# Kernel tuning notes

Hardware: AMD Instinct MI355X
Metric: run time of the kernel (lower is better)

The kernel has to match this reference:

```python
import jax, jax.numpy as jnp
import numpy as np

C = 256
G = 32  # groups
EPS = 1e-5

def _xavier(key, shape, gain=1.0):
    fan_in, fan_out = shape[1], shape[0]
    a = gain * np.sqrt(6.0 / (fan_in + fan_out))
    return jax.random.uniform(key, shape, jnp.float32, -a, a)

def setup_inputs() -> dict:
    key = jax.random.key(0)
    ks = jax.random.split(key, 5)
    x = jax.random.normal(ks[0], (2, C, 16, 16, 16), jnp.float32)
    return {
        "x": x,
        "gn_gamma": jnp.ones((C,), jnp.float32),
        "gn_beta": jnp.zeros((C,), jnp.float32),
        "Wq": _xavier(ks[1], (C, C)), "bq": jnp.zeros((C,), jnp.float32),
        "Wk": _xavier(ks[2], (C, C)), "bk": jnp.zeros((C,), jnp.float32),
        "Wv": _xavier(ks[3], (C, C)), "bv": jnp.zeros((C,), jnp.float32),
        "Wp": _xavier(ks[4], (C, C), gain=1e-05), "bp": jnp.zeros((C,), jnp.float32),
    }

def reference(x, gn_gamma, gn_beta, Wq, bq, Wk, bk, Wv, bv, Wp, bp):
    B, Cc, D, H, W = x.shape
    N = D * H * W
    xf = x.reshape(B, Cc, N)  # [B, C, N]
    # GroupNorm over (C//G, N) per group
    xg = xf.reshape(B, G, Cc // G, N)
    mu = jnp.mean(xg, axis=(2, 3), keepdims=True)
    var = jnp.var(xg, axis=(2, 3), keepdims=True)
    h = ((xg - mu) * jax.lax.rsqrt(var + EPS)).reshape(B, Cc, N)
    h = h * gn_gamma[None, :, None] + gn_beta[None, :, None]
    # 1x1x1 convs == channel matmuls
    q = jnp.einsum('oc,bcn->bno', Wq, h) + bq  # [B, N, C]
    k = jnp.einsum('oc,bcn->bon', Wk, h) + bk[None, :, None]  # [B, C, N]
    v = jnp.einsum('oc,bcn->bno', Wv, h) + bv  # [B, N, C]
    scale = float(Cc) ** (-0.5)
    w = jnp.einsum('bnc,bcm->bnm', q, k) * scale  # [B, N, N]
    w = jax.nn.softmax(w, axis=-1)
    a = jnp.einsum('bnm,bmc->bnc', w, v)  # [B, N, C]
    out = jnp.einsum('oc,bnc->bon', Wp, a) + bp[None, :, None]  # [B, C, N]
    return x + out.reshape(B, Cc, D, H, W)
```

## Files before the change

kernel.cpp:

```cpp
#include <hip/hip_runtime.h>
#include <stdint.h>

#define B_ 2
#define C_ 256
#define N_ 4096
#define EPS_ 1e-5f

typedef short short8 __attribute__((ext_vector_type(8)));
typedef float f32x4 __attribute__((ext_vector_type(4)));
typedef float f32x16 __attribute__((ext_vector_type(16)));
typedef long long i64;

static __device__ __forceinline__ unsigned short f2bf(float f) {
    union { float f; unsigned int u; } v; v.f = f;
    unsigned int r = v.u + 0x7FFF + ((v.u >> 16) & 1);
    return (unsigned short)(r >> 16);
}
static __device__ __forceinline__ float bf2f(unsigned short u) {
    union { unsigned int u; float f; } v; v.u = ((unsigned int)u) << 16;
    return v.f;
}
static __device__ __forceinline__ unsigned char f2fp8(float f) {
    return (unsigned char)(__builtin_amdgcn_cvt_pk_fp8_f32(f, f, 0, false) & 0xff);
}
static __device__ __forceinline__ unsigned short pk_bf8(float a, float b) {
    return (unsigned short)(__builtin_amdgcn_cvt_pk_bf8_f32(a, b, 0, false) & 0xffff);
}

__global__ __launch_bounds__(256) void prep(
    const float* __restrict__ x, float2* __restrict__ stats,
    const float* __restrict__ Wq, const float* __restrict__ Wk,
    const float* __restrict__ Wv, const float* __restrict__ Wp,
    ushort* __restrict__ o)
{
    __shared__ float as_[4], as2_[4];
    if (blockIdx.x < 64) {
        const float4* p = reinterpret_cast<const float4*>(x + (size_t)blockIdx.x * 32768);
        float s = 0.f, ss = 0.f;
        for (int i = threadIdx.x; i < 8192; i += 256) {
            float4 v = p[i];
            s  += v.x + v.y + v.z + v.w;
            ss += v.x*v.x + v.y*v.y + v.z*v.z + v.w*v.w;
        }
        for (int m = 32; m; m >>= 1) { s += __shfl_down(s, m, 64); ss += __shfl_down(ss, m, 64); }
        int w = threadIdx.x >> 6;
        if ((threadIdx.x & 63) == 0) { as_[w] = s; as2_[w] = ss; }
        __syncthreads();
        if (threadIdx.x == 0) {
            float S = as_[0]+as_[1]+as_[2]+as_[3], SS = as2_[0]+as2_[1]+as2_[2]+as2_[3];
            float mu = S / 32768.f;
            float var = SS / 32768.f - mu*mu;
            stats[blockIdx.x] = make_float2(mu, rsqrtf(var + EPS_));
        }
    } else {
        int t = (blockIdx.x - 64) * 256 + threadIdx.x;
        int idx = t * 4;
        int sel = idx >> 16;
        const float* src = sel == 0 ? Wq : sel == 1 ? Wk : sel == 2 ? Wv : Wp;
        float4 v = *reinterpret_cast<const float4*>(src + (idx & 65535));
        ushort4 r; r.x = f2bf(v.x); r.y = f2bf(v.y); r.z = f2bf(v.z); r.w = f2bf(v.w);
        *reinterpret_cast<ushort4*>(o + idx) = r;
    }
}

__global__ void gnorm_t(const float* __restrict__ x, const float2* __restrict__ stats,
                        const float* __restrict__ gamma, const float* __restrict__ beta,
                        ushort* __restrict__ ht) {
    __shared__ float tile[32][33];
    int b = blockIdx.z, n0 = blockIdx.x * 32, c0 = blockIdx.y * 32;
    int tx = threadIdx.x, ty = threadIdx.y;
    #pragma unroll
    for (int i = 0; i < 4; i++) {
        int c = c0 + ty + i*8;
        float2 st = stats[b*32 + (c >> 3)];
        float v = x[((size_t)(b*C_ + c))*N_ + n0 + tx];
        tile[ty + i*8][tx] = (v - st.x) * st.y * gamma[c] + beta[c];
    }
    __syncthreads();
    #pragma unroll
    for (int i = 0; i < 4; i++) {
        int n = n0 + ty + i*8;
        ht[((size_t)(b*N_ + n))*C_ + c0 + tx] = f2bf(tile[tx][ty + i*8]);
    }
}

__global__ __launch_bounds__(256) void qkvproj(
    const ushort* __restrict__ ht, const ushort* __restrict__ wq,
    const ushort* __restrict__ wk, const ushort* __restrict__ wv,
    const float* __restrict__ bq, const float* __restrict__ bk, const float* __restrict__ bv,
    unsigned char* __restrict__ qo, unsigned char* __restrict__ ko, unsigned char* __restrict__ vo)
{
    __shared__ ushort sA[64][72], sBq[64][72], sBk[64][72], sBv[64][72];
    int bz = blockIdx.z;
    const ushort* Ab = ht + (size_t)bz * N_ * C_;
    int i0 = blockIdx.x * 64, j0 = blockIdx.y * 64;
    int tid = threadIdx.x, w = tid >> 6, lane = tid & 63, lr = lane & 15, lg = lane >> 4;
    f32x4 aq[4] = {}, ak[4] = {}, av[4] = {};
    for (int ks = 0; ks < 256; ks += 64) {
        #pragma unroll
        for (int it = 0; it < 2; it++) {
            int ch = tid + it*256;
            int row = ch >> 3, cc = ch & 7;
            *reinterpret_cast<uint4*>(&sA[row][cc*8]) =
                *reinterpret_cast<const uint4*>(Ab + ((size_t)(i0 + row))*256 + ks + cc*8);
            *reinterpret_cast<uint4*>(&sBq[row][cc*8]) =
                *reinterpret_cast<const uint4*>(wq + ((size_t)(j0 + row))*256 + ks + cc*8);
            *reinterpret_cast<uint4*>(&sBk[row][cc*8]) =
                *reinterpret_cast<const uint4*>(wk + ((size_t)(j0 + row))*256 + ks + cc*8);
            *reinterpret_cast<uint4*>(&sBv[row][cc*8]) =
                *reinterpret_cast<const uint4*>(wv + ((size_t)(j0 + row))*256 + ks + cc*8);
        }
        __syncthreads();
        #pragma unroll
        for (int kc = 0; kc < 2; kc++) {
            short8 af = *reinterpret_cast<const short8*>(&sA[w*16 + lr][kc*32 + lg*8]);
            #pragma unroll
            for (int cb = 0; cb < 4; cb++) {
                short8 b1 = *reinterpret_cast<const short8*>(&sBq[cb*16 + lr][kc*32 + lg*8]);
                short8 b2 = *reinterpret_cast<const short8*>(&sBk[cb*16 + lr][kc*32 + lg*8]);
                short8 b3 = *reinterpret_cast<const short8*>(&sBv[cb*16 + lr][kc*32 + lg*8]);
                aq[cb] = __builtin_amdgcn_mfma_f32_16x16x32_bf16(af, b1, aq[cb], 0, 0, 0);
                ak[cb] = __builtin_amdgcn_mfma_f32_16x16x32_bf16(af, b2, ak[cb], 0, 0, 0);
                av[cb] = __builtin_amdgcn_mfma_f32_16x16x32_bf16(af, b3, av[cb], 0, 0, 0);
            }
        }
        __syncthreads();
    }
    #pragma unroll
    for (int cb = 0; cb < 4; cb++) {
        #pragma unroll
        for (int r = 0; r < 4; r++) {
            int i = i0 + w*16 + lg*4 + r;
            int j = j0 + cb*16 + lr;
            size_t oidx = ((size_t)(bz*N_ + i))*256 + j;
            qo[oidx] = f2fp8(aq[cb][r] + bq[j]);
            ko[oidx] = f2fp8(ak[cb][r] + bk[j]);
            int m = i & 63;
            int col = (i & ~63) + ((m & 31)*2 + (m >> 5));
            vo[((size_t)bz*C_ + j)*N_ + col] = f2fp8(av[cb][r] + bv[j]);
        }
    }
}

#define FLASH_LDS 79872
__global__ __launch_bounds__(256, 2) void flash5(
    const unsigned char* __restrict__ q, const unsigned char* __restrict__ k,
    const unsigned char* __restrict__ vT,
    ushort* __restrict__ Opart, float* __restrict__ lsum, ushort* __restrict__ aout, int nsplit)
{
    extern __shared__ char smem[];
    int b = blockIdx.z, s = blockIdx.y, qt = blockIdx.x;
    int tid = threadIdx.x, w = tid >> 6, lane = tid & 63;
    int l31 = lane & 31, hi = lane >> 5;
    int nrow0 = qt*128 + w*32;
    const unsigned char* kB = k  + (size_t)b * N_ * 256;
    const unsigned char* vB = vT + (size_t)b * 256 * N_;

    i64 qf[16];
    #pragma unroll
    for (int kc = 0; kc < 16; kc++)
        qf[kc] = *reinterpret_cast<const i64*>(
            q + ((size_t)(b*N_) + nrow0 + l31)*256 + kc*16 + hi*8);

    f32x16 oacc[8] = {};
    float lpart[16] = {};

    int tiles = 64 / nsplit;
    int t0 = s * tiles;

    char* kbuf0 = smem;
    char* vbuf0 = smem + 33792;
    char* pw    = smem + 70656 + w*2304;

    uint4 kreg[4], vreg[4];
    auto loadKV = [&](int t) {
        #pragma unroll
        for (int i = 0; i < 4; i++) {
            int row = w*16 + i*4 + (lane >> 4);
            kreg[i] = *reinterpret_cast<const uint4*>(
                kB + (size_t)(t*64 + row)*256 + (lane & 15)*16);
        }
        #pragma unroll
        for (int i = 0; i < 4; i++) {
            int c = w*64 + i*16 + (lane >> 2);
            vreg[i] = *reinterpret_cast<const uint4*>(
                vB + (size_t)c*4096 + t*64 + (lane & 3)*16);
        }
    };
    auto writeKV = [&](int sel) {
        #pragma unroll
        for (int i = 0; i < 4; i++) {
            int row = w*16 + i*4 + (lane >> 4);
            char* p = kbuf0 + sel*16896 + row*264 + (lane & 15)*16;
            *reinterpret_cast<uint2*>(p)     = make_uint2(kreg[i].x, kreg[i].y);
            *reinterpret_cast<uint2*>(p + 8) = make_uint2(kreg[i].z, kreg[i].w);
        }
        #pragma unroll
        for (int i = 0; i < 4; i++) {
            int c = w*64 + i*16 + (lane >> 2);
            char* p = vbuf0 + sel*18432 + c*72 + (lane & 3)*16;
            *reinterpret_cast<uint2*>(p)     = make_uint2(vreg[i].x, vreg[i].y);
            *reinterpret_cast<uint2*>(p + 8) = make_uint2(vreg[i].z, vreg[i].w);
        }
    };

    loadKV(t0);
    writeKV(0);
    __syncthreads();
    int sel = 0;

    for (int ti = 0; ti < tiles; ti++) {
        int t = t0 + ti;
        int tn = (ti + 1 < tiles) ? t + 1 : t0;
        loadKV(tn);

        const char* kb_ = kbuf0 + sel*16896;
        f32x16 s0 = {}, s1 = {};
        __builtin_amdgcn_s_setprio(1);
        #pragma unroll
        for (int kc = 0; kc < 16; kc++) {
            i64 b0 = *reinterpret_cast<const i64*>(kb_ + l31*264        + kc*16 + hi*8);
            i64 b1 = *reinterpret_cast<const i64*>(kb_ + (l31+32)*264   + kc*16 + hi*8);
            s0 = __builtin_amdgcn_mfma_f32_32x32x16_fp8_fp8(qf[kc], b0, s0, 0, 0, 0);
            s1 = __builtin_amdgcn_mfma_f32_32x32x16_fp8_fp8(qf[kc], b1, s1, 0, 0, 0);
        }
        __builtin_amdgcn_s_setprio(0);

        #pragma unroll
        for (int r = 0; r < 16; r++) {
            int R = (r & 3) + 8*(r >> 2) + 4*hi;
            float p0 = __expf(fminf(s0[r]*0.0625f, 10.5f));
            float p1 = __expf(fminf(s1[r]*0.0625f, 10.5f));
            lpart[r] += p0 + p1;
            *(ushort*)(pw + R*72 + l31*2) = pk_bf8(p0, p1);
        }

        const char* vb_ = vbuf0 + sel*18432;
        i64 pa[4];
        #pragma unroll
        for (int ks = 0; ks < 4; ks++)
            pa[ks] = *reinterpret_cast<const i64*>(pw + l31*72 + ks*16 + hi*8);
        __builtin_amdgcn_s_setprio(1);
        #pragma unroll
        for (int cb = 0; cb < 8; cb++) {
            #pragma unroll
            for (int ks = 0; ks < 4; ks++) {
                i64 bv = *reinterpret_cast<const i64*>(vb_ + (cb*32 + l31)*72 + ks*16 + hi*8);
                oacc[cb] = __builtin_amdgcn_mfma_f32_32x32x16_bf8_fp8(pa[ks], bv, oacc[cb], 0, 0, 0);
            }
        }
        __builtin_amdgcn_s_setprio(0);

        writeKV(sel ^ 1);
        __syncthreads();
        sel ^= 1;
    }

    #pragma unroll
    for (int r = 0; r < 16; r++) {
        float v = lpart[r];
        v += __shfl_xor(v, 1, 64);
        v += __shfl_xor(v, 2, 64);
        v += __shfl_xor(v, 4, 64);
        v += __shfl_xor(v, 8, 64);
        v += __shfl_xor(v, 16, 64);
        lpart[r] = v;
    }

    if (nsplit == 1) {
        #pragma unroll
        for (int r = 0; r < 16; r++) {
            int R = (r & 3) + 8*(r >> 2) + 4*hi;
            float inv = 1.f / lpart[r];
            #pragma unroll
            for (int cb = 0; cb < 8; cb++)
                aout[((size_t)(b*N_) + nrow0 + R)*256 + cb*32 + l31] = f2bf(oacc[cb][r] * inv);
        }
    } else {
        size_t obase = ((size_t)(b*nsplit + s)*N_ + nrow0) * 256;
        #pragma unroll
        for (int r = 0; r < 16; r++) {
            int R = (r & 3) + 8*(r >> 2) + 4*hi;
            #pragma unroll
            for (int cb = 0; cb < 8; cb++)
                Opart[obase + (size_t)R*256 + cb*32 + l31] = f2bf(oacc[cb][r]);
        }
        if (l31 == 0) {
            #pragma unroll
            for (int r = 0; r < 16; r++)
                lsum[(size_t)(b*nsplit + s)*N_ + nrow0 + (r & 3) + 8*(r >> 2) + 4*hi] = lpart[r];
        }
    }
}

__global__ void combine2(const ushort* __restrict__ Opart, const float* __restrict__ lsum,
                         ushort* __restrict__ aout, int nsplit) {
    int g = threadIdx.x >> 6, lane = threadIdx.x & 63;
    int idx = blockIdx.x*4 + g;
    int b = idx >> 12, n = idx & 4095;
    float L = 0.f;
    for (int s2 = 0; s2 < nsplit; s2++) L += lsum[(size_t)(b*nsplit + s2)*N_ + n];
    float inv = 1.f / L;
    float a0 = 0.f, a1 = 0.f, a2 = 0.f, a3 = 0.f;
    for (int s2 = 0; s2 < nsplit; s2++) {
        ushort4 o = *reinterpret_cast<const ushort4*>(
            Opart + ((size_t)(b*nsplit + s2)*N_ + n)*256 + lane*4);
        a0 += bf2f(o.x); a1 += bf2f(o.y); a2 += bf2f(o.z); a3 += bf2f(o.w);
    }
    ushort4 r; r.x = f2bf(a0*inv); r.y = f2bf(a1*inv); r.z = f2bf(a2*inv); r.w = f2bf(a3*inv);
    *reinterpret_cast<ushort4*>(aout + (size_t)idx*256 + lane*4) = r;
}

__global__ __launch_bounds__(256) void pgemm(
    const ushort* __restrict__ A, const ushort* __restrict__ Bm,
    const float* __restrict__ bias, const float* __restrict__ resid,
    float* __restrict__ outp, long bBatch, long oBatch)
{
    __shared__ ushort sA[64][72];
    __shared__ ushort sB[64][72];
    int bz = blockIdx.z;
    const ushort* Bb = Bm + (size_t)bBatch * bz;
    int i0 = blockIdx.x * 64, j0 = blockIdx.y * 64;
    int tid = threadIdx.x, w = tid >> 6, lane = tid & 63, lr = lane & 15, lg = lane >> 4;
    f32x4 acc[4] = {};
    for (int ks = 0; ks < 256; ks += 64) {
        #pragma unroll
        for (int it = 0; it < 2; it++) {
            int ch = tid + it*256;
            int row = ch >> 3, cc = ch & 7;
            *reinterpret_cast<uint4*>(&sA[row][cc*8]) =
                *reinterpret_cast<const uint4*>(A + ((size_t)(i0 + row))*256 + ks + cc*8);
            *reinterpret_cast<uint4*>(&sB[row][cc*8]) =
                *reinterpret_cast<const uint4*>(Bb + ((size_t)(j0 + row))*256 + ks + cc*8);
        }
        __syncthreads();
        #pragma unroll
        for (int kc = 0; kc < 2; kc++) {
            short8 af = *reinterpret_cast<const short8*>(&sA[w*16 + lr][kc*32 + lg*8]);
            #pragma unroll
            for (int cb = 0; cb < 4; cb++) {
                short8 bf = *reinterpret_cast<const short8*>(&sB[cb*16 + lr][kc*32 + lg*8]);
                acc[cb] = __builtin_amdgcn_mfma_f32_16x16x32_bf16(af, bf, acc[cb], 0, 0, 0);
            }
        }
        __syncthreads();
    }
    #pragma unroll
    for (int cb = 0; cb < 4; cb++) {
        #pragma unroll
        for (int r = 0; r < 4; r++) {
            int i = i0 + w*16 + lg*4 + r;
            int j = j0 + cb*16 + lr;
            size_t oidx = (size_t)oBatch*bz + (size_t)i*N_ + j;
            outp[oidx] = acc[cb][r] + bias[i] + resid[oidx];
        }
    }
}

extern "C" void kernel_launch(void* const* d_in, const int* in_sizes, int n_in,
                              void* d_out, int out_size, void* d_ws, size_t ws_size,
                              hipStream_t stream) {
    const float* x     = (const float*)d_in[0];
    const float* gamma = (const float*)d_in[1];
    const float* beta  = (const float*)d_in[2];
    const float* Wq = (const float*)d_in[3]; const float* bq = (const float*)d_in[4];
    const float* Wk = (const float*)d_in[5]; const float* bk = (const float*)d_in[6];
    const float* Wv = (const float*)d_in[7]; const float* bv = (const float*)d_in[8];
    const float* Wp = (const float*)d_in[9]; const float* bp = (const float*)d_in[10];
    float* out = (float*)d_out;

    char* ws = (char*)d_ws;
    float2* stats = (float2*)ws;
    ushort* wqb = (ushort*)(ws + 1024);
    ushort* wkb = wqb + 65536;
    ushort* wvb = wkb + 65536;
    ushort* wpb = wvb + 65536;
    ushort* ht  = (ushort*)(ws + 1024 + 524288);
    const size_t NB = (size_t)B_ * N_ * C_;
    unsigned char* qb  = (unsigned char*)(ht + NB);
    unsigned char* kb8 = qb  + NB;
    unsigned char* vTb = kb8 + NB;
    ushort* ab = (ushort*)(vTb + NB);
    char* after = (char*)(ab + NB);
    float*  lsum  = (float*)after;
    ushort* Opart = (ushort*)(after + 262144);

    int nsplit = (ws_size >= (size_t)48*1024*1024) ? 8 : 4;

    hipFuncSetAttribute((const void*)flash5, hipFuncAttributeMaxDynamicSharedMemorySize,
                        FLASH_LDS);

    prep<<<320, 256, 0, stream>>>(x, stats, Wq, Wk, Wv, Wp, wqb);
    gnorm_t<<<dim3(128, 8, 2), dim3(32, 8), 0, stream>>>(x, stats, gamma, beta, ht);
    qkvproj<<<dim3(64, 4, 2), 256, 0, stream>>>(ht, wqb, wkb, wvb, bq, bk, bv, qb, kb8, vTb);
    flash5<<<dim3(32, nsplit, 2), 256, FLASH_LDS, stream>>>(qb, kb8, vTb, Opart, lsum, ab, nsplit);
    combine2<<<2048, 256, 0, stream>>>(Opart, lsum, ab, nsplit);
    pgemm<<<dim3(4, 64, 2), 256, 0, stream>>>(wpb, ab, bp, x, out, (long)N_*C_, (long)C_*N_);
}
```

Before: 84.47 us.

## Use 32x32x64 scaled f8f6f4 MFMA in flash attention with permuted K LDS layout

```diff
diff --git a/kernel.cpp b/kernel.cpp
--- a/kernel.cpp
+++ b/kernel.cpp
@@ -9,6 +9,7 @@
 typedef short short8 __attribute__((ext_vector_type(8)));
 typedef float f32x4 __attribute__((ext_vector_type(4)));
 typedef float f32x16 __attribute__((ext_vector_type(16)));
+typedef int i32x8 __attribute__((ext_vector_type(8)));
 typedef long long i64;
 
 static __device__ __forceinline__ unsigned short f2bf(float f) {
@@ -26,6 +27,9 @@
 static __device__ __forceinline__ unsigned short pk_bf8(float a, float b) {
     return (unsigned short)(__builtin_amdgcn_cvt_pk_bf8_f32(a, b, 0, false) & 0xffff);
 }
+
+union U32B { uint4 q[2]; i32x8 v; };
+union U32C { uint2 d[4]; i32x8 v; };
 
 __global__ __launch_bounds__(256) void prep(
     const float* __restrict__ x, float2* __restrict__ stats,
@@ -135,15 +139,13 @@
             size_t oidx = ((size_t)(bz*N_ + i))*256 + j;
             qo[oidx] = f2fp8(aq[cb][r] + bq[j]);
             ko[oidx] = f2fp8(ak[cb][r] + bk[j]);
-            int m = i & 63;
-            int col = (i & ~63) + ((m & 31)*2 + (m >> 5));
-            vo[((size_t)bz*C_ + j)*N_ + col] = f2fp8(av[cb][r] + bv[j]);
-        }
-    }
-}
-
-#define FLASH_LDS 79872
-__global__ __launch_bounds__(256, 2) void flash5(
+            vo[((size_t)bz*C_ + j)*N_ + i] = f2fp8(av[cb][r] + bv[j]);
+        }
+    }
+}
+
+#define FLASH_LDS 80896
+__global__ __launch_bounds__(256, 2) void flash6(
     const unsigned char* __restrict__ q, const unsigned char* __restrict__ k,
     const unsigned char* __restrict__ vT,
     ushort* __restrict__ Opart, float* __restrict__ lsum, ushort* __restrict__ aout, int nsplit)
@@ -156,11 +158,11 @@
     const unsigned char* kB = k  + (size_t)b * N_ * 256;
     const unsigned char* vB = vT + (size_t)b * 256 * N_;
 
-    i64 qf[16];
-    #pragma unroll
-    for (int kc = 0; kc < 16; kc++)
-        qf[kc] = *reinterpret_cast<const i64*>(
-            q + ((size_t)(b*N_) + nrow0 + l31)*256 + kc*16 + hi*8);
+    i32x8 qf[4];
+    #pragma unroll
+    for (int ks = 0; ks < 4; ks++)
+        qf[ks] = *reinterpret_cast<const i32x8*>(
+            q + ((size_t)(b*N_) + nrow0 + l31)*256 + ks*64 + hi*32);
 
     f32x16 oacc[8] = {};
     float lpart[16] = {};
@@ -168,61 +170,60 @@
     int tiles = 64 / nsplit;
     int t0 = s * tiles;
 
-    char* kbuf0 = smem;
-    char* vbuf0 = smem + 33792;
-    char* pw    = smem + 70656 + w*2304;
+    char* kls = smem;
+    char* vls = smem + 34816;
+    char* pw  = smem + 71680 + w*2304;
+
+    int koff[4], kd[4], voff[4], vd[4];
+    #pragma unroll
+    for (int i = 0; i < 4; i++) {
+        int row = w*16 + i*4 + (lane >> 4);
+        koff[i] = (t0*64 + row)*256 + (lane & 15)*16;
+        int pr = (row & 1)*32 + (row >> 1);
+        kd[i]  = pr*272 + (lane & 15)*16;
+        int c = w*64 + i*16 + (lane >> 2);
+        voff[i] = c*4096 + t0*64 + (lane & 3)*16;
+        vd[i]   = c*72 + (lane & 3)*16;
+    }
 
     uint4 kreg[4], vreg[4];
-    auto loadKV = [&](int t) {
-        #pragma unroll
-        for (int i = 0; i < 4; i++) {
-            int row = w*16 + i*4 + (lane >> 4);
-            kreg[i] = *reinterpret_cast<const uint4*>(
-                kB + (size_t)(t*64 + row)*256 + (lane & 15)*16);
-        }
-        #pragma unroll
-        for (int i = 0; i < 4; i++) {
-            int c = w*64 + i*16 + (lane >> 2);
-            vreg[i] = *reinterpret_cast<const uint4*>(
-                vB + (size_t)c*4096 + t*64 + (lane & 3)*16);
-        }
+    auto loadKV = [&]() {
+        #pragma unroll
+        for (int i = 0; i < 4; i++) { kreg[i] = *reinterpret_cast<const uint4*>(kB + koff[i]); koff[i] += 16384; }
+        #pragma unroll
+        for (int i = 0; i < 4; i++) { vreg[i] = *reinterpret_cast<const uint4*>(vB + voff[i]); voff[i] += 64; }
     };
     auto writeKV = [&](int sel) {
         #pragma unroll
-        for (int i = 0; i < 4; i++) {
-            int row = w*16 + i*4 + (lane >> 4);
-            char* p = kbuf0 + sel*16896 + row*264 + (lane & 15)*16;
-            *reinterpret_cast<uint2*>(p)     = make_uint2(kreg[i].x, kreg[i].y);
-            *reinterpret_cast<uint2*>(p + 8) = make_uint2(kreg[i].z, kreg[i].w);
-        }
-        #pragma unroll
-        for (int i = 0; i < 4; i++) {
-            int c = w*64 + i*16 + (lane >> 2);
-            char* p = vbuf0 + sel*18432 + c*72 + (lane & 3)*16;
-            *reinterpret_cast<uint2*>(p)     = make_uint2(vreg[i].x, vreg[i].y);
-            *reinterpret_cast<uint2*>(p + 8) = make_uint2(vreg[i].z, vreg[i].w);
-        }
+        for (int i = 0; i < 4; i++) *reinterpret_cast<uint4*>(kls + sel*17408 + kd[i]) = kreg[i];
+        #pragma unroll
+        for (int i = 0; i < 4; i++) *reinterpret_cast<uint4*>(vls + sel*18432 + vd[i]) = vreg[i];
     };
 
-    loadKV(t0);
+    loadKV();
     writeKV(0);
     __syncthreads();
     int sel = 0;
 
     for (int ti = 0; ti < tiles; ti++) {
-        int t = t0 + ti;
-        int tn = (ti + 1 < tiles) ? t + 1 : t0;
-        loadKV(tn);
-
-        const char* kb_ = kbuf0 + sel*16896;
+        bool more = (ti + 1 < tiles);
+        if (more) loadKV();
+
+        const char* kb_ = kls + sel*17408;
         f32x16 s0 = {}, s1 = {};
         __builtin_amdgcn_s_setprio(1);
         #pragma unroll
-        for (int kc = 0; kc < 16; kc++) {
-            i64 b0 = *reinterpret_cast<const i64*>(kb_ + l31*264        + kc*16 + hi*8);
-            i64 b1 = *reinterpret_cast<const i64*>(kb_ + (l31+32)*264   + kc*16 + hi*8);
-            s0 = __builtin_amdgcn_mfma_f32_32x32x16_fp8_fp8(qf[kc], b0, s0, 0, 0, 0);
-            s1 = __builtin_amdgcn_mfma_f32_32x32x16_fp8_fp8(qf[kc], b1, s1, 0, 0, 0);
+        for (int ks = 0; ks < 4; ks++) {
+            int off = ks*64 + hi*32;
+            U32B b0, b1;
+            b0.q[0] = *reinterpret_cast<const uint4*>(kb_ + l31*272 + off);
+            b0.q[1] = *reinterpret_cast<const uint4*>(kb_ + l31*272 + off + 16);
+            b1.q[0] = *reinterpret_cast<const uint4*>(kb_ + (l31+32)*272 + off);
+            b1.q[1] = *reinterpret_cast<const uint4*>(kb_ + (l31+32)*272 + off + 16);
+            s0 = __builtin_amdgcn_mfma_scale_f32_32x32x64_f8f6f4(
+                     qf[ks], b0.v, s0, 0, 0, 0, 127, 0, 127);
+            s1 = __builtin_amdgcn_mfma_scale_f32_32x32x64_f8f6f4(
+                     qf[ks], b1.v, s1, 0, 0, 0, 127, 0, 127);
         }
         __builtin_amdgcn_s_setprio(0);
 
@@ -235,23 +236,27 @@
             *(ushort*)(pw + R*72 + l31*2) = pk_bf8(p0, p1);
         }
 
-        const char* vb_ = vbuf0 + sel*18432;
-        i64 pa[4];
-        #pragma unroll
-        for (int ks = 0; ks < 4; ks++)
-            pa[ks] = *reinterpret_cast<const i64*>(pw + l31*72 + ks*16 + hi*8);
+        U32C pa;
+        pa.d[0] = *reinterpret_cast<const uint2*>(pw + l31*72 + hi*32);
+        pa.d[1] = *reinterpret_cast<const uint2*>(pw + l31*72 + hi*32 + 8);
+        pa.d[2] = *reinterpret_cast<const uint2*>(pw + l31*72 + hi*32 + 16);
+        pa.d[3] = *reinterpret_cast<const uint2*>(pw + l31*72 + hi*32 + 24);
+        const char* vb_ = vls + sel*18432;
         __builtin_amdgcn_s_setprio(1);
         #pragma unroll
         for (int cb = 0; cb < 8; cb++) {
-            #pragma unroll
-            for (int ks = 0; ks < 4; ks++) {
-                i64 bv = *reinterpret_cast<const i64*>(vb_ + (cb*32 + l31)*72 + ks*16 + hi*8);
-                oacc[cb] = __builtin_amdgcn_mfma_f32_32x32x16_bf8_fp8(pa[ks], bv, oacc[cb], 0, 0, 0);
-            }
+            const char* pv = vb_ + (cb*32 + l31)*72 + hi*32;
+            U32C bv;
+            bv.d[0] = *reinterpret_cast<const uint2*>(pv);
+            bv.d[1] = *reinterpret_cast<const uint2*>(pv + 8);
+            bv.d[2] = *reinterpret_cast<const uint2*>(pv + 16);
+            bv.d[3] = *reinterpret_cast<const uint2*>(pv + 24);
+            oacc[cb] = __builtin_amdgcn_mfma_scale_f32_32x32x64_f8f6f4(
+                           pa.v, bv.v, oacc[cb], 1, 0, 0, 127, 0, 127);
         }
         __builtin_amdgcn_s_setprio(0);
 
-        writeKV(sel ^ 1);
+        if (more) writeKV(sel ^ 1);
         __syncthreads();
         sel ^= 1;
     }
@@ -387,13 +392,13 @@
 
     int nsplit = (ws_size >= (size_t)48*1024*1024) ? 8 : 4;
 
-    hipFuncSetAttribute((const void*)flash5, hipFuncAttributeMaxDynamicSharedMemorySize,
+    hipFuncSetAttribute((const void*)flash6, hipFuncAttributeMaxDynamicSharedMemorySize,
                         FLASH_LDS);
 
     prep<<<320, 256, 0, stream>>>(x, stats, Wq, Wk, Wv, Wp, wqb);
     gnorm_t<<<dim3(128, 8, 2), dim3(32, 8), 0, stream>>>(x, stats, gamma, beta, ht);
     qkvproj<<<dim3(64, 4, 2), 256, 0, stream>>>(ht, wqb, wkb, wvb, bq, bk, bv, qb, kb8, vTb);
-    flash5<<<dim3(32, nsplit, 2), 256, FLASH_LDS, stream>>>(qb, kb8, vTb, Opart, lsum, ab, nsplit);
+    flash6<<<dim3(32, nsplit, 2), 256, FLASH_LDS, stream>>>(qb, kb8, vTb, Opart, lsum, ab, nsplit);
     combine2<<<2048, 256, 0, stream>>>(Opart, lsum, ab, nsplit);
     pgemm<<<dim3(4, 64, 2), 256, 0, stream>>>(wpb, ab, bp, x, out, (long)N_*C_, (long)C_*N_);
 }
```

New measurement: 175.6 us. 108% more time.

## Rewrite flash attention with 16x16 MFMA tiles, direct-to-LDS K loads, single buffer

Applied to the files above, without the earlier changes.

```diff
diff --git a/kernel.cpp b/kernel.cpp
--- a/kernel.cpp
+++ b/kernel.cpp
@@ -8,7 +8,6 @@
 
 typedef short short8 __attribute__((ext_vector_type(8)));
 typedef float f32x4 __attribute__((ext_vector_type(4)));
-typedef float f32x16 __attribute__((ext_vector_type(16)));
 typedef long long i64;
 
 static __device__ __forceinline__ unsigned short f2bf(float f) {
@@ -23,8 +22,13 @@
 static __device__ __forceinline__ unsigned char f2fp8(float f) {
     return (unsigned char)(__builtin_amdgcn_cvt_pk_fp8_f32(f, f, 0, false) & 0xff);
 }
-static __device__ __forceinline__ unsigned short pk_bf8(float a, float b) {
-    return (unsigned short)(__builtin_amdgcn_cvt_pk_bf8_f32(a, b, 0, false) & 0xffff);
+static __device__ __forceinline__ unsigned char f2bf8(float f) {
+    return (unsigned char)(__builtin_amdgcn_cvt_pk_bf8_f32(f, f, 0, false) & 0xff);
+}
+static __device__ __forceinline__ void gll16(const void* g, void* l) {
+    __builtin_amdgcn_global_load_lds(
+        (const __attribute__((address_space(1))) unsigned int*)g,
+        (__attribute__((address_space(3))) unsigned int*)l, 16, 0, 0);
 }
 
 __global__ __launch_bounds__(256) void prep(
@@ -135,160 +139,162 @@
             size_t oidx = ((size_t)(bz*N_ + i))*256 + j;
             qo[oidx] = f2fp8(aq[cb][r] + bq[j]);
             ko[oidx] = f2fp8(ak[cb][r] + bk[j]);
-            int m = i & 63;
-            int col = (i & ~63) + ((m & 31)*2 + (m >> 5));
-            vo[((size_t)bz*C_ + j)*N_ + col] = f2fp8(av[cb][r] + bv[j]);
-        }
-    }
-}
-
-#define FLASH_LDS 79872
-__global__ __launch_bounds__(256, 2) void flash5(
+            vo[((size_t)bz*C_ + j)*N_ + i] = f2fp8(av[cb][r] + bv[j]);
+        }
+    }
+}
+
+#define FLASH_LDS 39424
+__global__ __launch_bounds__(256, 3) void flash8(
     const unsigned char* __restrict__ q, const unsigned char* __restrict__ k,
     const unsigned char* __restrict__ vT,
     ushort* __restrict__ Opart, float* __restrict__ lsum, ushort* __restrict__ aout, int nsplit)
 {
     extern __shared__ char smem[];
     int b = blockIdx.z, s = blockIdx.y, qt = blockIdx.x;
-    int tid = threadIdx.x, w = tid >> 6, lane = tid & 63;
-    int l31 = lane & 31, hi = lane >> 5;
-    int nrow0 = qt*128 + w*32;
+    int tid = threadIdx.x, w = tid >> 6, lane = tid & 63, lr = lane & 15, lg = lane >> 4;
+    int nrow0 = qt*64 + w*16;
     const unsigned char* kB = k  + (size_t)b * N_ * 256;
     const unsigned char* vB = vT + (size_t)b * 256 * N_;
 
-    i64 qf[16];
-    #pragma unroll
-    for (int kc = 0; kc < 16; kc++)
+    i64 qf[8];
+    #pragma unroll
+    for (int kc = 0; kc < 8; kc++)
         qf[kc] = *reinterpret_cast<const i64*>(
-            q + ((size_t)(b*N_) + nrow0 + l31)*256 + kc*16 + hi*8);
-
-    f32x16 oacc[8] = {};
-    float lpart[16] = {};
+            q + ((size_t)(b*N_) + nrow0 + lr)*256 + kc*32 + lg*8);
+
+    f32x4 oacc[16] = {};
+    float lpart[4] = {};
 
     int tiles = 64 / nsplit;
     int t0 = s * tiles;
 
-    char* kbuf0 = smem;
-    char* vbuf0 = smem + 33792;
-    char* pw    = smem + 70656 + w*2304;
-
-    uint4 kreg[4], vreg[4];
-    auto loadKV = [&](int t) {
+    char* kls = smem;
+    char* vls = smem + 16384;
+    char* pw  = smem + 34816 + w*1152;
+
+    int ksrc[4];
+    #pragma unroll
+    for (int i = 0; i < 4; i++) {
+        int c = w*4 + i;
+        int row = c*4 + (lane >> 4);
+        ksrc[i] = (t0*64 + row)*256 + (((lane & 15) ^ (row & 15)) << 4);
+    }
+    int voff[4], vd[4];
+    #pragma unroll
+    for (int i = 0; i < 4; i++) {
+        int c = w*64 + i*16 + (lane >> 2);
+        voff[i] = c*4096 + t0*64 + (lane & 3)*16;
+        vd[i]   = c*72 + (lane & 3)*16;
+    }
+
+    uint4 vreg[4];
+    auto loadV = [&]() {
+        #pragma unroll
+        for (int i = 0; i < 4; i++) { vreg[i] = *reinterpret_cast<const uint4*>(vB + voff[i]); voff[i] += 64; }
+    };
+    auto writeV = [&]() {
         #pragma unroll
         for (int i = 0; i < 4; i++) {
-            int row = w*16 + i*4 + (lane >> 4);
-            kreg[i] = *reinterpret_cast<const uint4*>(
-                kB + (size_t)(t*64 + row)*256 + (lane & 15)*16);
-        }
-        #pragma unroll
-        for (int i = 0; i < 4; i++) {
-            int c = w*64 + i*16 + (lane >> 2);
-            vreg[i] = *reinterpret_cast<const uint4*>(
-                vB + (size_t)c*4096 + t*64 + (lane & 3)*16);
-        }
-    };
-    auto writeKV = [&](int sel) {
-        #pragma unroll
-        for (int i = 0; i < 4; i++) {
-            int row = w*16 + i*4 + (lane >> 4);
-            char* p = kbuf0 + sel*16896 + row*264 + (lane & 15)*16;
-            *reinterpret_cast<uint2*>(p)     = make_uint2(kreg[i].x, kreg[i].y);
-            *reinterpret_cast<uint2*>(p + 8) = make_uint2(kreg[i].z, kreg[i].w);
-        }
-        #pragma unroll
-        for (int i = 0; i < 4; i++) {
-            int c = w*64 + i*16 + (lane >> 2);
-            char* p = vbuf0 + sel*18432 + c*72 + (lane & 3)*16;
+            char* p = vls + vd[i];
             *reinterpret_cast<uint2*>(p)     = make_uint2(vreg[i].x, vreg[i].y);
             *reinterpret_cast<uint2*>(p + 8) = make_uint2(vreg[i].z, vreg[i].w);
         }
     };
-
-    loadKV(t0);
-    writeKV(0);
+    auto stageK = [&]() {
+        #pragma unroll
+        for (int i = 0; i < 4; i++) {
+            gll16(kB + ksrc[i], kls + (w*4 + i)*1024);
+            ksrc[i] += 16384;
+        }
+    };
+
+    loadV();
+    stageK();
+    writeV();
     __syncthreads();
-    int sel = 0;
 
     for (int ti = 0; ti < tiles; ti++) {
-        int t = t0 + ti;
-        int tn = (ti + 1 < tiles) ? t + 1 : t0;
-        loadKV(tn);
-
-        const char* kb_ = kbuf0 + sel*16896;
-        f32x16 s0 = {}, s1 = {};
+        bool more = (ti + 1 < tiles);
+        if (more) loadV();
+
+        f32x4 sacc[4] = {};
         __builtin_amdgcn_s_setprio(1);
         #pragma unroll
-        for (int kc = 0; kc < 16; kc++) {
-            i64 b0 = *reinterpret_cast<const i64*>(kb_ + l31*264        + kc*16 + hi*8);
-            i64 b1 = *reinterpret_cast<const i64*>(kb_ + (l31+32)*264   + kc*16 + hi*8);
-            s0 = __builtin_amdgcn_mfma_f32_32x32x16_fp8_fp8(qf[kc], b0, s0, 0, 0, 0);
-            s1 = __builtin_amdgcn_mfma_f32_32x32x16_fp8_fp8(qf[kc], b1, s1, 0, 0, 0);
+        for (int kc = 0; kc < 8; kc++) {
+            int c2 = kc*2 + (lg >> 1);
+            #pragma unroll
+            for (int cb = 0; cb < 4; cb++) {
+                int row = cb*16 + lr;
+                i64 bf = *reinterpret_cast<const i64*>(
+                    kls + row*256 + ((c2 ^ (row & 15)) << 4) + (lg & 1)*8);
+                sacc[cb] = __builtin_amdgcn_mfma_f32_16x16x32_fp8_fp8(qf[kc], bf, sacc[cb], 0, 0, 0);
+            }
         }
         __builtin_amdgcn_s_setprio(0);
 
         #pragma unroll
-        for (int r = 0; r < 16; r++) {
-            int R = (r & 3) + 8*(r >> 2) + 4*hi;
-            float p0 = __expf(fminf(s0[r]*0.0625f, 10.5f));
-            float p1 = __expf(fminf(s1[r]*0.0625f, 10.5f));
-            lpart[r] += p0 + p1;
-            *(ushort*)(pw + R*72 + l31*2) = pk_bf8(p0, p1);
-        }
-
-        const char* vb_ = vbuf0 + sel*18432;
-        i64 pa[4];
-        #pragma unroll
-        for (int ks = 0; ks < 4; ks++)
-            pa[ks] = *reinterpret_cast<const i64*>(pw + l31*72 + ks*16 + hi*8);
+        for (int cb = 0; cb < 4; cb++) {
+            #pragma unroll
+            for (int r = 0; r < 4; r++) {
+                float e = __expf(fminf(sacc[cb][r]*0.0625f, 10.5f));
+                lpart[r] += e;
+                *(unsigned char*)(pw + (lg*4 + r)*72 + cb*16 + lr) = f2bf8(e);
+            }
+        }
+
+        i64 pa0 = *reinterpret_cast<const i64*>(pw + lr*72 + lg*8);
+        i64 pa1 = *reinterpret_cast<const i64*>(pw + lr*72 + 32 + lg*8);
         __builtin_amdgcn_s_setprio(1);
         #pragma unroll
-        for (int cb = 0; cb < 8; cb++) {
-            #pragma unroll
-            for (int ks = 0; ks < 4; ks++) {
-                i64 bv = *reinterpret_cast<const i64*>(vb_ + (cb*32 + l31)*72 + ks*16 + hi*8);
-                oacc[cb] = __builtin_amdgcn_mfma_f32_32x32x16_bf8_fp8(pa[ks], bv, oacc[cb], 0, 0, 0);
-            }
+        for (int cb = 0; cb < 16; cb++) {
+            const char* vrow = vls + (cb*16 + lr)*72;
+            i64 bv0 = *reinterpret_cast<const i64*>(vrow + lg*8);
+            oacc[cb] = __builtin_amdgcn_mfma_f32_16x16x32_bf8_fp8(pa0, bv0, oacc[cb], 0, 0, 0);
+            i64 bv1 = *reinterpret_cast<const i64*>(vrow + 32 + lg*8);
+            oacc[cb] = __builtin_amdgcn_mfma_f32_16x16x32_bf8_fp8(pa1, bv1, oacc[cb], 0, 0, 0);
         }
         __builtin_amdgcn_s_setprio(0);
 
-        writeKV(sel ^ 1);
-        __syncthreads();
-        sel ^= 1;
-    }
-
-    #pragma unroll
-    for (int r = 0; r < 16; r++) {
+        if (more) {
+            __syncthreads();
+            stageK();
+            writeV();
+            __syncthreads();
+        }
+    }
+
+    #pragma unroll
+    for (int r = 0; r < 4; r++) {
         float v = lpart[r];
         v += __shfl_xor(v, 1, 64);
         v += __shfl_xor(v, 2, 64);
         v += __shfl_xor(v, 4, 64);
         v += __shfl_xor(v, 8, 64);
-        v += __shfl_xor(v, 16, 64);
         lpart[r] = v;
     }
 
     if (nsplit == 1) {
         #pragma unroll
-        for (int r = 0; r < 16; r++) {
-            int R = (r & 3) + 8*(r >> 2) + 4*hi;
+        for (int r = 0; r < 4; r++) {
             float inv = 1.f / lpart[r];
-            #pragma unroll
-            for (int cb = 0; cb < 8; cb++)
-                aout[((size_t)(b*N_) + nrow0 + R)*256 + cb*32 + l31] = f2bf(oacc[cb][r] * inv);
+            int n = nrow0 + lg*4 + r;
+            #pragma unroll
+            for (int cb = 0; cb < 16; cb++)
+                aout[((size_t)(b*N_) + n)*256 + cb*16 + lr] = f2bf(oacc[cb][r] * inv);
         }
     } else {
         size_t obase = ((size_t)(b*nsplit + s)*N_ + nrow0) * 256;
         #pragma unroll
-        for (int r = 0; r < 16; r++) {
-            int R = (r & 3) + 8*(r >> 2) + 4*hi;
-            #pragma unroll
-            for (int cb = 0; cb < 8; cb++)
-                Opart[obase + (size_t)R*256 + cb*32 + l31] = f2bf(oacc[cb][r]);
-        }
-        if (l31 == 0) {
-            #pragma unroll
-            for (int r = 0; r < 16; r++)
-                lsum[(size_t)(b*nsplit + s)*N_ + nrow0 + (r & 3) + 8*(r >> 2) + 4*hi] = lpart[r];
+        for (int r = 0; r < 4; r++) {
+            #pragma unroll
+            for (int cb = 0; cb < 16; cb++)
+                Opart[obase + (size_t)(lg*4 + r)*256 + cb*16 + lr] = f2bf(oacc[cb][r]);
+        }
+        if (lr == 0) {
+            #pragma unroll
+            for (int r = 0; r < 4; r++)
+                lsum[(size_t)(b*nsplit + s)*N_ + nrow0 + lg*4 + r] = lpart[r];
         }
     }
 }
@@ -387,13 +393,13 @@
 
     int nsplit = (ws_size >= (size_t)48*1024*1024) ? 8 : 4;
 
-    hipFuncSetAttribute((const void*)flash5, hipFuncAttributeMaxDynamicSharedMemorySize,
+    hipFuncSetAttribute((const void*)flash8, hipFuncAttributeMaxDynamicSharedMemorySize,
                         FLASH_LDS);
 
     prep<<<320, 256, 0, stream>>>(x, stats, Wq, Wk, Wv, Wp, wqb);
     gnorm_t<<<dim3(128, 8, 2), dim3(32, 8), 0, stream>>>(x, stats, gamma, beta, ht);
     qkvproj<<<dim3(64, 4, 2), 256, 0, stream>>>(ht, wqb, wkb, wvb, bq, bk, bv, qb, kb8, vTb);
-    flash5<<<dim3(32, nsplit, 2), 256, FLASH_LDS, stream>>>(qb, kb8, vTb, Opart, lsum, ab, nsplit);
+    flash8<<<dim3(64, nsplit, 2), 256, FLASH_LDS, stream>>>(qb, kb8, vTb, Opart, lsum, ab, nsplit);
     combine2<<<2048, 256, 0, stream>>>(Opart, lsum, ab, nsplit);
     pgemm<<<dim3(4, 64, 2), 256, 0, stream>>>(wpb, ab, bp, x, out, (long)N_*C_, (long)C_*N_);
 }
```

New measurement: 104.6 us. +23.8%, slower.

## Restructure flash attention into 512-thread blocks with 32-key tiles and 16-way split

Applied to the files above, without the earlier changes.

```diff
diff --git a/kernel.cpp b/kernel.cpp
--- a/kernel.cpp
+++ b/kernel.cpp
@@ -5,6 +5,7 @@
 #define C_ 256
 #define N_ 4096
 #define EPS_ 1e-5f
+#define NSPLIT 16
 
 typedef short short8 __attribute__((ext_vector_type(8)));
 typedef float f32x4 __attribute__((ext_vector_type(4)));
@@ -23,8 +24,8 @@
 static __device__ __forceinline__ unsigned char f2fp8(float f) {
     return (unsigned char)(__builtin_amdgcn_cvt_pk_fp8_f32(f, f, 0, false) & 0xff);
 }
-static __device__ __forceinline__ unsigned short pk_bf8(float a, float b) {
-    return (unsigned short)(__builtin_amdgcn_cvt_pk_bf8_f32(a, b, 0, false) & 0xffff);
+static __device__ __forceinline__ unsigned char f2bf8(float f) {
+    return (unsigned char)(__builtin_amdgcn_cvt_pk_bf8_f32(f, f, 0, false) & 0xff);
 }
 
 __global__ __launch_bounds__(256) void prep(
@@ -135,24 +136,21 @@
             size_t oidx = ((size_t)(bz*N_ + i))*256 + j;
             qo[oidx] = f2fp8(aq[cb][r] + bq[j]);
             ko[oidx] = f2fp8(ak[cb][r] + bk[j]);
-            int m = i & 63;
-            int col = (i & ~63) + ((m & 31)*2 + (m >> 5));
-            vo[((size_t)bz*C_ + j)*N_ + col] = f2fp8(av[cb][r] + bv[j]);
-        }
-    }
-}
-
-#define FLASH_LDS 79872
-__global__ __launch_bounds__(256, 2) void flash5(
+            vo[((size_t)bz*C_ + j)*N_ + i] = f2fp8(av[cb][r] + bv[j]);
+        }
+    }
+}
+
+__global__ __launch_bounds__(512, 4) void flash9(
     const unsigned char* __restrict__ q, const unsigned char* __restrict__ k,
     const unsigned char* __restrict__ vT,
-    ushort* __restrict__ Opart, float* __restrict__ lsum, ushort* __restrict__ aout, int nsplit)
+    unsigned char* __restrict__ Opart, float* __restrict__ lsum)
 {
-    extern __shared__ char smem[];
+    __shared__ __align__(16) char smem[47616];
     int b = blockIdx.z, s = blockIdx.y, qt = blockIdx.x;
     int tid = threadIdx.x, w = tid >> 6, lane = tid & 63;
     int l31 = lane & 31, hi = lane >> 5;
-    int nrow0 = qt*128 + w*32;
+    int nrow0 = qt*256 + w*32;
     const unsigned char* kB = k  + (size_t)b * N_ * 256;
     const unsigned char* vB = vT + (size_t)b * 256 * N_;
 
@@ -165,64 +163,50 @@
     f32x16 oacc[8] = {};
     float lpart[16] = {};
 
-    int tiles = 64 / nsplit;
+    const int tiles = 128 / NSPLIT;
     int t0 = s * tiles;
 
-    char* kbuf0 = smem;
-    char* vbuf0 = smem + 33792;
-    char* pw    = smem + 70656 + w*2304;
-
-    uint4 kreg[4], vreg[4];
-    auto loadKV = [&](int t) {
-        #pragma unroll
-        for (int i = 0; i < 4; i++) {
-            int row = w*16 + i*4 + (lane >> 4);
-            kreg[i] = *reinterpret_cast<const uint4*>(
-                kB + (size_t)(t*64 + row)*256 + (lane & 15)*16);
-        }
-        #pragma unroll
-        for (int i = 0; i < 4; i++) {
-            int c = w*64 + i*16 + (lane >> 2);
-            vreg[i] = *reinterpret_cast<const uint4*>(
-                vB + (size_t)c*4096 + t*64 + (lane & 3)*16);
-        }
+    char* kls = smem;
+    char* vls = smem + 16896;
+    char* pw  = smem + 37376 + w*1280;
+
+    int krow = tid >> 4, kchunk = tid & 15;
+    int vc = tid >> 1, vhalf = tid & 1;
+    int ksrc = (t0*32 + krow)*256 + kchunk*16;
+    int kdst = krow*264 + kchunk*16;
+    int vsrc = vc*4096 + t0*32 + vhalf*16;
+    int vdst = vc*40 + vhalf*16;
+
+    uint4 kreg, vreg;
+    auto loadKV = [&]() {
+        kreg = *reinterpret_cast<const uint4*>(kB + ksrc); ksrc += 8192;
+        vreg = *reinterpret_cast<const uint4*>(vB + vsrc); vsrc += 32;
     };
     auto writeKV = [&](int sel) {
-        #pragma unroll
-        for (int i = 0; i < 4; i++) {
-            int row = w*16 + i*4 + (lane >> 4);
-            char* p = kbuf0 + sel*16896 + row*264 + (lane & 15)*16;
-            *reinterpret_cast<uint2*>(p)     = make_uint2(kreg[i].x, kreg[i].y);
-            *reinterpret_cast<uint2*>(p + 8) = make_uint2(kreg[i].z, kreg[i].w);
-        }
-        #pragma unroll
-        for (int i = 0; i < 4; i++) {
-            int c = w*64 + i*16 + (lane >> 2);
-            char* p = vbuf0 + sel*18432 + c*72 + (lane & 3)*16;
-            *reinterpret_cast<uint2*>(p)     = make_uint2(vreg[i].x, vreg[i].y);
-            *reinterpret_cast<uint2*>(p + 8) = make_uint2(vreg[i].z, vreg[i].w);
-        }
+        char* pk = kls + sel*8448 + kdst;
+        *reinterpret_cast<uint2*>(pk)     = make_uint2(kreg.x, kreg.y);
+        *reinterpret_cast<uint2*>(pk + 8) = make_uint2(kreg.z, kreg.w);
+        char* pv = vls + sel*10240 + vdst;
+        *reinterpret_cast<uint2*>(pv)     = make_uint2(vreg.x, vreg.y);
+        *reinterpret_cast<uint2*>(pv + 8) = make_uint2(vreg.z, vreg.w);
     };
 
-    loadKV(t0);
+    loadKV();
     writeKV(0);
     __syncthreads();
     int sel = 0;
 
     for (int ti = 0; ti < tiles; ti++) {
-        int t = t0 + ti;
-        int tn = (ti + 1 < tiles) ? t + 1 : t0;
-        loadKV(tn);
-
-        const char* kb_ = kbuf0 + sel*16896;
-        f32x16 s0 = {}, s1 = {};
+        bool more = (ti + 1 < tiles);
+        if (more) loadKV();
+
+        const char* kb_ = kls + sel*8448;
+        f32x16 s0 = {};
         __builtin_amdgcn_s_setprio(1);
         #pragma unroll
         for (int kc = 0; kc < 16; kc++) {
-            i64 b0 = *reinterpret_cast<const i64*>(kb_ + l31*264        + kc*16 + hi*8);
-            i64 b1 = *reinterpret_cast<const i64*>(kb_ + (l31+32)*264   + kc*16 + hi*8);
-            s0 = __builtin_amdgcn_mfma_f32_32x32x16_fp8_fp8(qf[kc], b0, s0, 0, 0, 0);
-            s1 = __builtin_amdgcn_mfma_f32_32x32x16_fp8_fp8(qf[kc], b1, s1, 0, 0, 0);
+            i64 bf = *reinterpret_cast<const i64*>(kb_ + l31*264 + kc*16 + hi*8);
+            s0 = __builtin_amdgcn_mfma_f32_32x32x16_fp8_fp8(qf[kc], bf, s0, 0, 0, 0);
         }
         __builtin_amdgcn_s_setprio(0);
 
@@ -230,30 +214,29 @@
         for (int r = 0; r < 16; r++) {
             int R = (r & 3) + 8*(r >> 2) + 4*hi;
             float p0 = __expf(fminf(s0[r]*0.0625f, 10.5f));
-            float p1 = __expf(fminf(s1[r]*0.0625f, 10.5f));
-            lpart[r] += p0 + p1;
-            *(ushort*)(pw + R*72 + l31*2) = pk_bf8(p0, p1);
-        }
-
-        const char* vb_ = vbuf0 + sel*18432;
-        i64 pa[4];
-        #pragma unroll
-        for (int ks = 0; ks < 4; ks++)
-            pa[ks] = *reinterpret_cast<const i64*>(pw + l31*72 + ks*16 + hi*8);
+            lpart[r] += p0;
+            *(unsigned char*)(pw + R*40 + l31) = f2bf8(p0);
+        }
+
+        i64 pa0 = *reinterpret_cast<const i64*>(pw + l31*40 + hi*8);
+        i64 pa1 = *reinterpret_cast<const i64*>(pw + l31*40 + 16 + hi*8);
+        const char* vb_ = vls + sel*10240;
         __builtin_amdgcn_s_setprio(1);
         #pragma unroll
         for (int cb = 0; cb < 8; cb++) {
-            #pragma unroll
-            for (int ks = 0; ks < 4; ks++) {
-                i64 bv = *reinterpret_cast<const i64*>(vb_ + (cb*32 + l31)*72 + ks*16 + hi*8);
-                oacc[cb] = __builtin_amdgcn_mfma_f32_32x32x16_bf8_fp8(pa[ks], bv, oacc[cb], 0, 0, 0);
-            }
+            const char* vrow = vb_ + (cb*32 + l31)*40;
+            i64 bv0 = *reinterpret_cast<const i64*>(vrow + hi*8);
+            oacc[cb] = __builtin_amdgcn_mfma_f32_32x32x16_bf8_fp8(pa0, bv0, oacc[cb], 0, 0, 0);
+            i64 bv1 = *reinterpret_cast<const i64*>(vrow + 16 + hi*8);
+            oacc[cb] = __builtin_amdgcn_mfma_f32_32x32x16_bf8_fp8(pa1, bv1, oacc[cb], 0, 0, 0);
         }
         __builtin_amdgcn_s_setprio(0);
 
-        writeKV(sel ^ 1);
-        __syncthreads();
-        sel ^= 1;
+        if (more) {
+            writeKV(sel ^ 1);
+            __syncthreads();
+            sel ^= 1;
+        }
     }
 
     #pragma unroll
@@ -267,45 +250,39 @@
         lpart[r] = v;
     }
 
-    if (nsplit == 1) {
-        #pragma unroll
-        for (int r = 0; r < 16; r++) {
-            int R = (r & 3) + 8*(r >> 2) + 4*hi;
-            float inv = 1.f / lpart[r];
-            #pragma unroll
-            for (int cb = 0; cb < 8; cb++)
-                aout[((size_t)(b*N_) + nrow0 + R)*256 + cb*32 + l31] = f2bf(oacc[cb][r] * inv);
-        }
-    } else {
-        size_t obase = ((size_t)(b*nsplit + s)*N_ + nrow0) * 256;
-        #pragma unroll
-        for (int r = 0; r < 16; r++) {
-            int R = (r & 3) + 8*(r >> 2) + 4*hi;
-            #pragma unroll
-            for (int cb = 0; cb < 8; cb++)
-                Opart[obase + (size_t)R*256 + cb*32 + l31] = f2bf(oacc[cb][r]);
-        }
-        if (l31 == 0) {
-            #pragma unroll
-            for (int r = 0; r < 16; r++)
-                lsum[(size_t)(b*nsplit + s)*N_ + nrow0 + (r & 3) + 8*(r >> 2) + 4*hi] = lpart[r];
-        }
-    }
-}
-
-__global__ void combine2(const ushort* __restrict__ Opart, const float* __restrict__ lsum,
-                         ushort* __restrict__ aout, int nsplit) {
+    size_t obase = ((size_t)(b*NSPLIT + s)*N_ + nrow0) * 256;
+    #pragma unroll
+    for (int r = 0; r < 16; r++) {
+        int R = (r & 3) + 8*(r >> 2) + 4*hi;
+        #pragma unroll
+        for (int cb = 0; cb < 8; cb++)
+            Opart[obase + (size_t)R*256 + cb*32 + l31] = f2bf8(oacc[cb][r]);
+    }
+    if (l31 == 0) {
+        #pragma unroll
+        for (int r = 0; r < 16; r++)
+            lsum[(size_t)(b*NSPLIT + s)*N_ + nrow0 + (r & 3) + 8*(r >> 2) + 4*hi] = lpart[r];
+    }
+}
+
+__global__ void combine3(const unsigned char* __restrict__ Opart, const float* __restrict__ lsum,
+                         ushort* __restrict__ aout) {
     int g = threadIdx.x >> 6, lane = threadIdx.x & 63;
     int idx = blockIdx.x*4 + g;
     int b = idx >> 12, n = idx & 4095;
     float L = 0.f;
-    for (int s2 = 0; s2 < nsplit; s2++) L += lsum[(size_t)(b*nsplit + s2)*N_ + n];
+    #pragma unroll
+    for (int s2 = 0; s2 < NSPLIT; s2++) L += lsum[(size_t)(b*NSPLIT + s2)*N_ + n];
     float inv = 1.f / L;
     float a0 = 0.f, a1 = 0.f, a2 = 0.f, a3 = 0.f;
-    for (int s2 = 0; s2 < nsplit; s2++) {
-        ushort4 o = *reinterpret_cast<const ushort4*>(
-            Opart + ((size_t)(b*nsplit + s2)*N_ + n)*256 + lane*4);
-        a0 += bf2f(o.x); a1 += bf2f(o.y); a2 += bf2f(o.z); a3 += bf2f(o.w);
+    #pragma unroll
+    for (int s2 = 0; s2 < NSPLIT; s2++) {
+        unsigned int o = *reinterpret_cast<const unsigned int*>(
+            Opart + ((size_t)(b*NSPLIT + s2)*N_ + n)*256 + lane*4);
+        a0 += __builtin_amdgcn_cvt_f32_bf8((int)o, 0);
+        a1 += __builtin_amdgcn_cvt_f32_bf8((int)o, 1);
+        a2 += __builtin_amdgcn_cvt_f32_bf8((int)o, 2);
+        a3 += __builtin_amdgcn_cvt_f32_bf8((int)o, 3);
     }
     ushort4 r; r.x = f2bf(a0*inv); r.y = f2bf(a1*inv); r.z = f2bf(a2*inv); r.w = f2bf(a3*inv);
     *reinterpret_cast<ushort4*>(aout + (size_t)idx*256 + lane*4) = r;
@@ -382,18 +359,13 @@
     unsigned char* vTb = kb8 + NB;
     ushort* ab = (ushort*)(vTb + NB);
     char* after = (char*)(ab + NB);
-    float*  lsum  = (float*)after;
-    ushort* Opart = (ushort*)(after + 262144);
-
-    int nsplit = (ws_size >= (size_t)48*1024*1024) ? 8 : 4;
-
-    hipFuncSetAttribute((const void*)flash5, hipFuncAttributeMaxDynamicSharedMemorySize,
-                        FLASH_LDS);
+    float* lsum = (float*)after;
+    unsigned char* Opart = (unsigned char*)(after + 524288);
 
     prep<<<320, 256, 0, stream>>>(x, stats, Wq, Wk, Wv, Wp, wqb);
     gnorm_t<<<dim3(128, 8, 2), dim3(32, 8), 0, stream>>>(x, stats, gamma, beta, ht);
     qkvproj<<<dim3(64, 4, 2), 256, 0, stream>>>(ht, wqb, wkb, wvb, bq, bk, bv, qb, kb8, vTb);
-    flash5<<<dim3(32, nsplit, 2), 256, FLASH_LDS, stream>>>(qb, kb8, vTb, Opart, lsum, ab, nsplit);
-    combine2<<<2048, 256, 0, stream>>>(Opart, lsum, ab, nsplit);
+    flash9<<<dim3(16, NSPLIT, 2), 512, 0, stream>>>(qb, kb8, vTb, Opart, lsum);
+    combine3<<<2048, 256, 0, stream>>>(Opart, lsum, ab);
     pgemm<<<dim3(4, 64, 2), 256, 0, stream>>>(wpb, ab, bp, x, out, (long)N_*C_, (long)C_*N_);
 }
```

After: 287.7 us. 241% more time.
